# Optimization experiments

Measured on AMD Instinct MI355X. Metric: run time of the kernel, lower is better.

Reference implementation:

```python
import jax, jax.numpy as jnp
import numpy as np

N_P, N_W, F_IN = 512, 3584, 256
H1, O1 = 8, 32
H2, O2 = 8, 256
BATCH = 1024
NEG_SLOPE = 0.2


def _xavier(key, shape):
    fan_in, fan_out = shape[-2], shape[-1]
    lim = jnp.sqrt(6.0 / (fan_in + fan_out))
    return jax.random.uniform(key, shape, jnp.float32, -lim, lim)


def setup_inputs() -> dict:
    key = jax.random.key(0)
    ks = jax.random.split(key, 16)
    return {
        "input": jax.random.uniform(ks[0], (BATCH, N_W), jnp.float32),
        "pern_feature": jax.random.normal(ks[1], (N_P, F_IN), jnp.float32),
        "word_feature": jax.random.normal(ks[2], (N_W, F_IN), jnp.float32),
        "w1": _xavier(ks[3], (H1, F_IN, O1)),
        "a_src1": _xavier(ks[4], (H1, O1, 1)),
        "a_dst1": _xavier(ks[5], (H1, O1, 1)),
        "b1": jnp.zeros((O1,), jnp.float32),
        "w2": _xavier(ks[6], (H2, F_IN, O2)),
        "a_src2": _xavier(ks[7], (H2, F_IN, 1)),
        "a_dst2": _xavier(ks[8], (H2, F_IN, 1)),
        "b2": jnp.zeros((O2,), jnp.float32),
        "W_fc": _xavier(ks[9], (O2, 5)),
        "b_fc": jnp.zeros((5,), jnp.float32),
        "pern_adj": jax.random.randint(ks[10], (N_P, N_P), 0, 2, jnp.int32),
        "word_pern_adj": jax.random.randint(ks[11], (N_P + N_W, N_P + N_W), 0, 2, jnp.int32),
    }


def gat(h, adj, w, a_src, a_dst, bias):
    # h: [N, f_in], adj: [N, N] int, w: [H, f_in, f_out]
    h_prime = jnp.einsum('nf,hfo->hno', h, w)          # [H, N, O]
    t = jnp.tanh(h_prime)
    s_src = jnp.einsum('hno,hoi->hn', t, a_src)        # [H, N]
    s_dst = jnp.einsum('hno,hoi->hn', t, a_dst)        # [H, N]
    attn = s_src[:, :, None] + s_dst[:, None, :]       # [H, N, N]
    attn = jnp.where(attn >= 0, attn, NEG_SLOPE * attn)  # leaky_relu
    attn = jnp.where(adj[None, :, :] > 0, attn, -jnp.inf)
    attn = jax.nn.softmax(attn, axis=-1)
    out = jnp.einsum('hnm,hmo->hno', attn, h_prime)    # [H, N, O]
    return out + bias


def reference(input, pern_feature, word_feature, w1, a_src1, a_dst1, b1,
              w2, a_src2, a_dst2, b2, W_fc, b_fc, pern_adj, word_pern_adj):
    n_p = pern_feature.shape[0]
    # GAT 1 over personality graph
    h1 = gat(pern_feature, pern_adj, w1, a_src1, a_dst1, b1)       # [H1, n_p, O1]
    hiddn_pp = jnp.transpose(h1, (1, 0, 2)).reshape(n_p, -1)        # [n_p, H1*O1]
    hiddn_pp = jax.nn.elu(hiddn_pp)
    # dropout is identity in eval mode
    hiddn_wp = jnp.concatenate([word_feature, hiddn_pp], axis=0)    # [N, 256]
    h2 = gat(hiddn_wp, word_pern_adj, w2, a_src2, a_dst2, b2)       # [H2, N, O2]
    hiddn_wp2 = h2.mean(axis=0)                                     # [N, O2]
    hiddn_w = hiddn_wp2[:word_feature.shape[0], :]                  # [n_w, O2]
    x = (input @ hiddn_w) / input.sum(axis=1, keepdims=True)        # [B, O2]
    return x @ W_fc + b_fc                                          # [B, 5]
```

## Files before the change

### kernel.cpp

```cpp
#include <hip/hip_runtime.h>
#include <hip/hip_bf16.h>
#include <math.h>

#define NP 512
#define NW 3584
#define NT 4096
#define FIN 256
#define H1 8
#define O1 32
#define H2 8
#define O2 256
#define NEG 0.2f

typedef __attribute__((ext_vector_type(8))) short bf16x8;
typedef __attribute__((ext_vector_type(4))) float f32x4;
typedef __attribute__((ext_vector_type(2))) float v2f;
typedef unsigned long long u64;

__device__ __forceinline__ unsigned short f2bf(float f) {
    unsigned u = __float_as_uint(f);
    unsigned r = (u + 0x7FFF + ((u >> 16) & 1)) >> 16;
    return (unsigned short)r;
}
__device__ __forceinline__ float bf2f(unsigned short s) {
    return __uint_as_float(((unsigned)s) << 16);
}

__global__ __launch_bounds__(256) void k_prep(
    const float* __restrict__ wf, const float* __restrict__ pf,
    const float* __restrict__ w1, const float* __restrict__ a_src1,
    const float* __restrict__ a_dst1, const float* __restrict__ w2,
    const float* __restrict__ b2, const float* __restrict__ W_fc,
    const int* __restrict__ wp_adj,
    unsigned short* __restrict__ abf, unsigned short* __restrict__ btbf,
    float* __restrict__ hp1, float* __restrict__ ss1, float* __restrict__ sd1,
    u64* __restrict__ maskT64, float* __restrict__ cvec)
{
    __shared__ float tile[64][65];
    __shared__ float feat[2][FIN];
    __shared__ float red[4][5];
    int blk = blockIdx.x;
    int t = threadIdx.x;
    if (blk < 896) {
        int idx4 = blk * 256 + t;
        float4 x = ((const float4*)wf)[idx4];
        ushort4 y;
        y.x = f2bf(x.x); y.y = f2bf(x.y); y.z = f2bf(x.z); y.w = f2bf(x.w);
        ((ushort4*)abf)[idx4] = y;
    } else if (blk < 1152) {
        int n0 = (blk - 896) * 2;
        feat[0][t] = pf[n0 * FIN + t];
        feat[1][t] = pf[(n0 + 1) * FIN + t];
        __syncthreads();
        int h = t >> 5, o = t & 31;
        float acc0 = 0.f, acc1 = 0.f;
        const float* wcol = w1 + h * FIN * O1 + o;
        #pragma unroll 4
        for (int f = 0; f < FIN; f++) {
            float w = wcol[f * O1];
            acc0 += feat[0][f] * w;
            acc1 += feat[1][f] * w;
        }
        hp1[n0 * 256 + t] = acc0;
        hp1[(n0 + 1) * 256 + t] = acc1;
        float as = a_src1[h * O1 + o];
        float ad = a_dst1[h * O1 + o];
        float accs[2] = {acc0, acc1};
        #pragma unroll
        for (int i = 0; i < 2; i++) {
            float th = tanhf(accs[i]);
            float vs = th * as, vd = th * ad;
            #pragma unroll
            for (int off = 1; off < 32; off <<= 1) {
                vs += __shfl_xor(vs, off);
                vd += __shfl_xor(vd, off);
            }
            if (o == 0) { ss1[h * NP + n0 + i] = vs; sd1[h * NP + n0 + i] = vd; }
        }
    } else if (blk < 1280) {
        int blk2 = blk - 1152;
        int h = blk2 >> 4;
        int f0 = ((blk2 >> 2) & 3) * 64;
        int o0 = (blk2 & 3) * 64;
        #pragma unroll
        for (int rr = 0; rr < 16; rr++) {
            int f = rr * 4 + (t >> 6);
            int o = t & 63;
            tile[f][o] = w2[((size_t)(h * FIN + f0 + f)) * O2 + o0 + o];
        }
        __syncthreads();
        #pragma unroll
        for (int rr = 0; rr < 16; rr++) {
            int o = rr * 4 + (t >> 6);
            int f = t & 63;
            btbf[((size_t)(h * O2 + o0 + o)) * FIN + f0 + f] = f2bf(tile[f][o]);
        }
    } else if (blk < 2176) {
        int w = t >> 6, l = t & 63;
        int r = (blk - 1280) * 4 + w;
        const int4* row = (const int4*)(wp_adj + (size_t)r * NT);
        for (int c4 = 0; c4 < 16; c4++) {
            int4 x = row[c4 * 64 + l];
            u64 nib = (u64)((x.x != 0 ? 1 : 0) | (x.y != 0 ? 2 : 0) |
                            (x.z != 0 ? 4 : 0) | (x.w != 0 ? 8 : 0));
            u64 v = nib << (4 * (l & 15));
            v |= __shfl_xor(v, 1);
            v |= __shfl_xor(v, 2);
            v |= __shfl_xor(v, 4);
            v |= __shfl_xor(v, 8);
            if ((l & 15) == 0) {
                int qw = c4 * 4 + (l >> 4);
                maskT64[(size_t)qw * NW + r] = v;
            }
        }
    } else {
        float v[5];
        #pragma unroll
        for (int j = 0; j < 5; j++) v[j] = b2[t] * W_fc[t * 5 + j];
        #pragma unroll
        for (int off = 1; off < 64; off <<= 1)
            #pragma unroll
            for (int j = 0; j < 5; j++) v[j] += __shfl_xor(v[j], off);
        int w = t >> 6, l = t & 63;
        if (l == 0) { for (int j = 0; j < 5; j++) red[w][j] = v[j]; }
        __syncthreads();
        if (t == 0)
            for (int j = 0; j < 5; j++) cvec[j] = red[0][j] + red[1][j] + red[2][j] + red[3][j];
    }
}

__global__ __launch_bounds__(256) void k_gat1_attn(
    const int* __restrict__ adj, const float* __restrict__ hp1,
    const float* __restrict__ ss1, const float* __restrict__ sd1,
    const float* __restrict__ b1, unsigned short* __restrict__ abf)
{
    __shared__ float p[2][H1][NP];
    __shared__ float den[2][H1];
    int t = threadIdx.x;
    int n0 = blockIdx.x * 2;
    for (int rr = 0; rr < 32; rr++) {
        int idx = rr * 256 + t;
        int i = idx >> 12, h = (idx >> 9) & 7, m = idx & 511;
        float a = adj[(n0 + i) * NP + m] > 0 ? 1.0f : 0.0f;
        float e = ss1[h * NP + n0 + i] + sd1[h * NP + m];
        e = fmaxf(e, NEG * e);
        p[i][h][m] = a * __expf(e);
    }
    __syncthreads();
    int w = t >> 6, l = t & 63;
    {
        int i = w & 1;
        #pragma unroll
        for (int hh = 0; hh < 4; hh++) {
            int h = (w >> 1) * 4 + hh;
            float s = 0;
            #pragma unroll
            for (int q = 0; q < 8; q++) s += p[i][h][l + 64 * q];
            #pragma unroll
            for (int off = 1; off < 64; off <<= 1) s += __shfl_xor(s, off);
            if (l == 0) den[i][h] = s;
        }
    }
    __syncthreads();
    int h = t >> 5, o = t & 31;
    float a0a = 0.f, a0b = 0.f, a1a = 0.f, a1b = 0.f;
    #pragma unroll 8
    for (int m = 0; m < NP; m += 2) {
        float v0 = hp1[m * 256 + t];
        float v1 = hp1[(m + 1) * 256 + t];
        a0a += p[0][h][m] * v0;
        a1a += p[1][h][m] * v0;
        a0b += p[0][h][m + 1] * v1;
        a1b += p[1][h][m + 1] * v1;
    }
    float acc[2] = {a0a + a0b, a1a + a1b};
    float bo = b1[o];
    #pragma unroll
    for (int i = 0; i < 2; i++) {
        float r = acc[i] / den[i][h] + bo;
        r = r > 0.f ? r : expm1f(r);
        abf[(NW + n0 + i) * FIN + t] = f2bf(r);
    }
}

__global__ __launch_bounds__(256) void k_gemm_hp2(
    const unsigned short* __restrict__ abf, const unsigned short* __restrict__ btbf,
    unsigned short* __restrict__ hp2T)
{
    __shared__ unsigned short As[64][264];
    int b = blockIdx.x;
    int h = b & 7, mt = b >> 3;
    int t = threadIdx.x;
    int w = t >> 6, l = t & 63;
    int m0 = mt * 64;
    {
        int row = t >> 5;
        int col8 = (t & 31) * 8;
        #pragma unroll
        for (int u = 0; u < 8; u++)
            *(bf16x8*)(&As[u * 8 + row][col8]) =
                *(const bf16x8*)(abf + (size_t)(m0 + u * 8 + row) * FIN + col8);
    }
    __syncthreads();
    int n0 = w * 64;
    int lr = l & 15, lq = l >> 4;
    const unsigned short* bbase = btbf + h * O2 * FIN;
    f32x4 acc[4][4];
    #pragma unroll
    for (int i = 0; i < 4; i++)
        #pragma unroll
        for (int j = 0; j < 4; j++) acc[i][j] = (f32x4){0.f, 0.f, 0.f, 0.f};
    #pragma unroll
    for (int k = 0; k < FIN; k += 32) {
        bf16x8 a[4], bf[4];
        int kc = k + lq * 8;
        #pragma unroll
        for (int j = 0; j < 4; j++)
            bf[j] = *(const bf16x8*)(bbase + (size_t)(n0 + j * 16 + lr) * FIN + kc);
        #pragma unroll
        for (int i = 0; i < 4; i++)
            a[i] = *(const bf16x8*)(&As[i * 16 + lr][kc]);
        #pragma unroll
        for (int i = 0; i < 4; i++)
            #pragma unroll
            for (int j = 0; j < 4; j++)
                acc[i][j] = __builtin_amdgcn_mfma_f32_16x16x32_bf16(bf[j], a[i], acc[i][j], 0, 0, 0);
    }
    #pragma unroll
    for (int i = 0; i < 4; i++)
        #pragma unroll
        for (int j = 0; j < 4; j++)
            #pragma unroll
            for (int r = 0; r < 4; r++) {
                int o = n0 + j * 16 + lq * 4 + r;
                hp2T[((size_t)h * O2 + o) * NT + m0 + i * 16 + lr] = f2bf(acc[i][j][r]);
            }
}

__global__ __launch_bounds__(256) void k_reduce(
    const unsigned short* __restrict__ hp2T,
    const float* __restrict__ a_src2, const float* __restrict__ a_dst2,
    const float* __restrict__ W_fc, float* __restrict__ gpart)
{
    int b = blockIdx.x;
    int cs = b & 3, mb = (b >> 2) & 15, h = b >> 6;
    int m = mb * 256 + threadIdx.x;
    float s[7] = {0,0,0,0,0,0,0};
    const unsigned short* base = hp2T + ((size_t)h * O2 + cs * 64) * NT + m;
    #pragma unroll 8
    for (int oi = 0; oi < 64; oi++) {
        int o = cs * 64 + oi;
        float x = bf2f(base[(size_t)oi * NT]);
        float ex = __expf(2.0f * x);
        float th = 1.0f - 2.0f * __builtin_amdgcn_rcpf(ex + 1.0f);
        s[0] += th * a_src2[h * O2 + o];
        s[1] += th * a_dst2[h * O2 + o];
        #pragma unroll
        for (int jj = 0; jj < 5; jj++) s[2 + jj] += x * W_fc[o * 5 + jj];
    }
    float* dst = gpart + (((size_t)(h * 4 + cs)) * NT + m) * 8;
    float4 d0 = {s[0], s[1], s[2], s[3]};
    float4 d1 = {s[4], s[5], s[6], 0.f};
    *(float4*)dst = d0;
    *(float4*)(dst + 4) = d1;
}

__global__ __launch_bounds__(256) void k_comb_hp2(
    const float* __restrict__ gpart,
    float* __restrict__ Etab, float* __restrict__ Eptab, float* __restrict__ T)
{
    int idx = blockIdx.x * 256 + threadIdx.x;
    float s[7] = {0,0,0,0,0,0,0};
    #pragma unroll
    for (int sl = 0; sl < 4; sl++) {
        const float* p = gpart + (((size_t)(idx >> 12) * 4 + sl) * NT + (idx & (NT - 1))) * 8;
        #pragma unroll
        for (int q = 0; q < 7; q++) s[q] += p[q];
    }
    Etab[idx]  = __expf(s[0]);
    Eptab[idx] = __expf(NEG * s[0]);
    float4 t0 = {__expf(s[1]), __expf(NEG * s[1]), 1.0f, s[2]};
    float4 t1 = {s[3], s[4], s[5], s[6]};
    *(float4*)(T + (size_t)idx * 8)     = t0;
    *(float4*)(T + (size_t)idx * 8 + 4) = t1;
}

__global__ __launch_bounds__(256) void k_gat2_attn(
    const u64* __restrict__ maskT64, const float* __restrict__ Etab,
    const float* __restrict__ Eptab, const float* __restrict__ T,
    float* __restrict__ part)
{
    int t = threadIdx.x;
    int w = t >> 6, l = t & 63;
    int b = blockIdx.x;
    int nb = b % 112;
    int h  = (b / 112) & 7;
    int c  = b / 896;
    int n0 = __builtin_amdgcn_readfirstlane(nb * 32 + w * 8);
    u64 epk[8];
    #pragma unroll
    for (int i = 0; i < 8; i++) {
        int r = h * NT + n0 + i;
        unsigned e  = __builtin_amdgcn_readfirstlane(__float_as_uint(Etab[r]));
        unsigned ep = __builtin_amdgcn_readfirstlane(__float_as_uint(Eptab[r]));
        epk[i] = ((u64)ep << 32) | e;
    }
    float den[8] = {0,0,0,0,0,0,0,0};
    float num[8][5] = {{0}};
    const float* Th = T + ((size_t)h * NT + c * 2048) * 8;
    for (int q = 0; q < 32; q++) {
        const float* tp = Th + (size_t)(q * 64 + l) * 8;
        f32x4 t0 = *(const f32x4*)tp;
        f32x4 t1 = *(const f32x4*)(tp + 4);
        v2f ffp = {t0.x, t0.y};
        size_t moff = (size_t)(c * 32 + q) * NW + n0;
        const u64* mq = maskT64 + moff;
        #pragma unroll
        for (int i = 0; i < 8; i++) {
            u64 wv = mq[i];
            unsigned wlo = __builtin_amdgcn_readfirstlane((unsigned)wv);
            unsigned whi = __builtin_amdgcn_readfirstlane((unsigned)(wv >> 32));
            u64 word = ((u64)whi << 32) | wlo;
            v2f pab;
            asm("v_pk_mul_f32 %0, %1, %2" : "=v"(pab) : "v"(ffp), "s"(epk[i]));
            float pp0 = fmaxf(pab.x, pab.y);
            float pp;
            asm("v_cndmask_b32 %0, 0, %1, %2" : "=v"(pp) : "v"(pp0), "s"(word));
            den[i] += pp;
            num[i][0] = fmaf(pp, t0.w, num[i][0]);
            num[i][1] = fmaf(pp, t1.x, num[i][1]);
            num[i][2] = fmaf(pp, t1.y, num[i][2]);
            num[i][3] = fmaf(pp, t1.z, num[i][3]);
            num[i][4] = fmaf(pp, t1.w, num[i][4]);
        }
    }
    #pragma unroll
    for (int i = 0; i < 8; i++) {
        float v[6];
        v[0] = den[i];
        #pragma unroll
        for (int j = 0; j < 5; j++) v[1 + j] = num[i][j];
        #pragma unroll
        for (int off = 1; off < 8; off <<= 1)
            #pragma unroll
            for (int k = 0; k < 6; k++) v[k] += __shfl_xor(v[k], off);
        if ((l & 7) == 0) {
            float* dst = part + ((((size_t)c * NW + n0 + i) * 8 + h) * 8 + (l >> 3)) * 8;
            #pragma unroll
            for (int k = 0; k < 6; k++) dst[k] = v[k];
        }
    }
}

__global__ __launch_bounds__(256) void k_gat2_comb(const float* __restrict__ part,
                                                   float* __restrict__ hf) {
    int idx = blockIdx.x * 256 + threadIdx.x;
    int n = idx >> 3, h = idx & 7;
    float den = 0, num[5] = {0,0,0,0,0};
    #pragma unroll
    for (int cc = 0; cc < 2; cc++) {
        #pragma unroll
        for (int s = 0; s < 8; s++) {
            const float* p = part + ((((size_t)cc * NW + n) * 8 + h) * 8 + s) * 8;
            float4 a = *(const float4*)p;
            float4 bq = *(const float4*)(p + 4);
            den += a.x;
            num[0] += a.y; num[1] += a.z; num[2] += a.w;
            num[3] += bq.x; num[4] += bq.y;
        }
    }
    float inv = 1.0f / (den * 8.0f);
    float v[5];
    #pragma unroll
    for (int j = 0; j < 5; j++) v[j] = num[j] * inv;
    #pragma unroll
    for (int off = 1; off < 8; off <<= 1)
        #pragma unroll
        for (int j = 0; j < 5; j++) v[j] += __shfl_xor(v[j], off);
    if (h == 0) {
        #pragma unroll
        for (int j = 0; j < 5; j++) hf[n * 5 + j] = v[j];
    }
}

__global__ __launch_bounds__(256) void k_final(
    const float* __restrict__ input, const float* __restrict__ hf,
    const float* __restrict__ cvec, const float* __restrict__ b_fc,
    float* __restrict__ out)
{
    int b = blockIdx.x, t = threadIdx.x;
    const float4* row4 = (const float4*)(input + (size_t)b * NW);
    const float4* hf4 = (const float4*)hf;
    float s = 0.f, a[5] = {0.f, 0.f, 0.f, 0.f, 0.f};
    for (int idx = t; idx < NW / 4; idx += 256) {
        float4 x = row4[idx];
        float f[20];
        #pragma unroll
        for (int q = 0; q < 5; q++) *(float4*)(f + 4 * q) = hf4[idx * 5 + q];
        s += x.x + x.y + x.z + x.w;
        #pragma unroll
        for (int j = 0; j < 5; j++)
            a[j] += x.x * f[j] + x.y * f[5 + j] + x.z * f[10 + j] + x.w * f[15 + j];
    }
    #pragma unroll
    for (int off = 1; off < 64; off <<= 1) {
        s += __shfl_xor(s, off);
        #pragma unroll
        for (int j = 0; j < 5; j++) a[j] += __shfl_xor(a[j], off);
    }
    __shared__ float red[4][6];
    int w = t >> 6, l = t & 63;
    if (l == 0) { red[w][0] = s; for (int j = 0; j < 5; j++) red[w][j + 1] = a[j]; }
    __syncthreads();
    if (t < 5) {
        float st = red[0][0] + red[1][0] + red[2][0] + red[3][0];
        float aj = red[0][t + 1] + red[1][t + 1] + red[2][t + 1] + red[3][t + 1];
        out[b * 5 + t] = aj / st + cvec[t] + b_fc[t];
    }
}

extern "C" void kernel_launch(void* const* d_in, const int* in_sizes, int n_in,
                              void* d_out, int out_size, void* d_ws, size_t ws_size,
                              hipStream_t stream) {
    const float* input   = (const float*)d_in[0];
    const float* pf      = (const float*)d_in[1];
    const float* wf      = (const float*)d_in[2];
    const float* w1      = (const float*)d_in[3];
    const float* a_src1  = (const float*)d_in[4];
    const float* a_dst1  = (const float*)d_in[5];
    const float* b1      = (const float*)d_in[6];
    const float* w2      = (const float*)d_in[7];
    const float* a_src2  = (const float*)d_in[8];
    const float* a_dst2  = (const float*)d_in[9];
    const float* b2      = (const float*)d_in[10];
    const float* W_fc    = (const float*)d_in[11];
    const float* b_fc    = (const float*)d_in[12];
    const int* pern_adj  = (const int*)d_in[13];
    const int* wp_adj    = (const int*)d_in[14];
    float* out = (float*)d_out;

    char* ws = (char*)d_ws;
    unsigned short* abf    = (unsigned short*)(ws);
    unsigned short* btbf   = (unsigned short*)(ws + 2097152);
    float*          hp1    = (float*)(ws + 3145728);
    float*          ss1    = (float*)(ws + 3670016);
    float*          sd1    = (float*)(ws + 3686400);
    float*          Etab   = (float*)(ws + 3833856);
    float*          Eptab  = (float*)(ws + 3964928);
    float*          T      = (float*)(ws + 4096000);
    float*          hf     = (float*)(ws + 5144576);
    float*          cvec   = (float*)(ws + 5216256);
    u64*            maskT64= (u64*)(ws + 5216512);
    float*          gpart  = (float*)(ws + 7051520);
    unsigned short* hp2T   = (unsigned short*)(ws + 11245824);
    float*          part   = (float*)(ws + 11245824);

    k_prep<<<2177, 256, 0, stream>>>(wf, pf, w1, a_src1, a_dst1, w2, b2, W_fc,
                                     wp_adj, abf, btbf, hp1, ss1, sd1, maskT64, cvec);
    k_gat1_attn<<<256, 256, 0, stream>>>(pern_adj, hp1, ss1, sd1, b1, abf);
    k_gemm_hp2<<<512, 256, 0, stream>>>(abf, btbf, hp2T);
    k_reduce<<<512, 256, 0, stream>>>(hp2T, a_src2, a_dst2, W_fc, gpart);
    k_comb_hp2<<<128, 256, 0, stream>>>(gpart, Etab, Eptab, T);
    k_gat2_attn<<<1792, 256, 0, stream>>>(maskT64, Etab, Eptab, T, part);
    k_gat2_comb<<<112, 256, 0, stream>>>(part, hf);
    k_final<<<1024, 256, 0, stream>>>(input, hf, cvec, b_fc, out);
}
```

Before: 250.7 us.

## Fuse tanh/score reduction into GEMM epilogue and stage adjacency mask in LDS

The separate k_reduce pass is folded into the hp2 GEMM epilogue. The epilogue computes the tanh attention scores and the W_fc projections straight from the MFMA accumulators, which drops the bf16 hp2T round trip through global memory and one kernel launch. A small weight table packs a_src2, a_dst2 and W_fc per output column. The GAT2 attention kernel now reads the adjacency mask as 32-bit words staged in shared memory, extracting bits per lane instead of using readfirstlane and an inline-asm cndmask on 64-bit words. This adds some shuffle reductions in the epilogue, and per-lane bit extraction costs extra VALU work in the hot loop.

Measured after the change: 248.3 us. About the same (-1.0%).

```diff
diff --git a/kernel.cpp b/kernel.cpp
--- a/kernel.cpp
+++ b/kernel.cpp
@@ -14,7 +14,6 @@
 
 typedef __attribute__((ext_vector_type(8))) short bf16x8;
 typedef __attribute__((ext_vector_type(4))) float f32x4;
-typedef __attribute__((ext_vector_type(2))) float v2f;
 typedef unsigned long long u64;
 
 __device__ __forceinline__ unsigned short f2bf(float f) {
@@ -22,8 +21,8 @@
     unsigned r = (u + 0x7FFF + ((u >> 16) & 1)) >> 16;
     return (unsigned short)r;
 }
-__device__ __forceinline__ float bf2f(unsigned short s) {
-    return __uint_as_float(((unsigned)s) << 16);
+__device__ __forceinline__ float rflf(float x) {
+    return __uint_as_float(__builtin_amdgcn_readfirstlane(__float_as_uint(x)));
 }
 
 __global__ __launch_bounds__(256) void k_prep(
@@ -31,10 +30,12 @@
     const float* __restrict__ w1, const float* __restrict__ a_src1,
     const float* __restrict__ a_dst1, const float* __restrict__ w2,
     const float* __restrict__ b2, const float* __restrict__ W_fc,
+    const float* __restrict__ a_src2, const float* __restrict__ a_dst2,
     const int* __restrict__ wp_adj,
     unsigned short* __restrict__ abf, unsigned short* __restrict__ btbf,
     float* __restrict__ hp1, float* __restrict__ ss1, float* __restrict__ sd1,
-    u64* __restrict__ maskT64, float* __restrict__ cvec)
+    unsigned* __restrict__ maskT, float* __restrict__ cvec,
+    float* __restrict__ wtab)
 {
     __shared__ float tile[64][65];
     __shared__ float feat[2][FIN];
@@ -110,10 +111,11 @@
             v |= __shfl_xor(v, 8);
             if ((l & 15) == 0) {
                 int qw = c4 * 4 + (l >> 4);
-                maskT64[(size_t)qw * NW + r] = v;
+                maskT[(size_t)(2 * qw) * NW + r]     = (unsigned)v;
+                maskT[(size_t)(2 * qw + 1) * NW + r] = (unsigned)(v >> 32);
             }
         }
-    } else {
+    } else if (blk == 2176) {
         float v[5];
         #pragma unroll
         for (int j = 0; j < 5; j++) v[j] = b2[t] * W_fc[t * 5 + j];
@@ -126,6 +128,14 @@
         __syncthreads();
         if (t == 0)
             for (int j = 0; j < 5; j++) cvec[j] = red[0][j] + red[1][j] + red[2][j] + red[3][j];
+    } else {
+        int h = blk - 2177;
+        int o = t;
+        float* dst = wtab + ((size_t)h * O2 + o) * 8;
+        float4 d0 = {a_src2[h * O2 + o], a_dst2[h * O2 + o], W_fc[o * 5], W_fc[o * 5 + 1]};
+        float4 d1 = {W_fc[o * 5 + 2], W_fc[o * 5 + 3], W_fc[o * 5 + 4], 0.f};
+        *(float4*)dst = d0;
+        *(float4*)(dst + 4) = d1;
     }
 }
 
@@ -185,7 +195,7 @@
 
 __global__ __launch_bounds__(256) void k_gemm_hp2(
     const unsigned short* __restrict__ abf, const unsigned short* __restrict__ btbf,
-    unsigned short* __restrict__ hp2T)
+    const float* __restrict__ wtab, float* __restrict__ gpart)
 {
     __shared__ unsigned short As[64][264];
     int b = blockIdx.x;
@@ -226,43 +236,42 @@
             for (int j = 0; j < 4; j++)
                 acc[i][j] = __builtin_amdgcn_mfma_f32_16x16x32_bf16(bf[j], a[i], acc[i][j], 0, 0, 0);
     }
-    #pragma unroll
-    for (int i = 0; i < 4; i++)
-        #pragma unroll
-        for (int j = 0; j < 4; j++)
+    const float* wt = wtab + (size_t)h * O2 * 8;
+    float* base = gpart + ((size_t)h * 4 + w) * NT * 8;
+    #pragma unroll
+    for (int i = 0; i < 4; i++) {
+        float s[7] = {0,0,0,0,0,0,0};
+        #pragma unroll
+        for (int j = 0; j < 4; j++) {
             #pragma unroll
             for (int r = 0; r < 4; r++) {
-                int o = n0 + j * 16 + lq * 4 + r;
-                hp2T[((size_t)h * O2 + o) * NT + m0 + i * 16 + lr] = f2bf(acc[i][j][r]);
+                float x = acc[i][j][r];
+                float ex = __expf(2.0f * x);
+                float th = 1.0f - 2.0f * __builtin_amdgcn_rcpf(ex + 1.0f);
+                const float* wp = wt + (size_t)(n0 + j * 16 + lq * 4 + r) * 8;
+                float4 wa = *(const float4*)wp;
+                float4 wb = *(const float4*)(wp + 4);
+                s[0] += th * wa.x;
+                s[1] += th * wa.y;
+                s[2] += x * wa.z;
+                s[3] += x * wa.w;
+                s[4] += x * wb.x;
+                s[5] += x * wb.y;
+                s[6] += x * wb.z;
             }
-}
-
-__global__ __launch_bounds__(256) void k_reduce(
-    const unsigned short* __restrict__ hp2T,
-    const float* __restrict__ a_src2, const float* __restrict__ a_dst2,
-    const float* __restrict__ W_fc, float* __restrict__ gpart)
-{
-    int b = blockIdx.x;
-    int cs = b & 3, mb = (b >> 2) & 15, h = b >> 6;
-    int m = mb * 256 + threadIdx.x;
-    float s[7] = {0,0,0,0,0,0,0};
-    const unsigned short* base = hp2T + ((size_t)h * O2 + cs * 64) * NT + m;
-    #pragma unroll 8
-    for (int oi = 0; oi < 64; oi++) {
-        int o = cs * 64 + oi;
-        float x = bf2f(base[(size_t)oi * NT]);
-        float ex = __expf(2.0f * x);
-        float th = 1.0f - 2.0f * __builtin_amdgcn_rcpf(ex + 1.0f);
-        s[0] += th * a_src2[h * O2 + o];
-        s[1] += th * a_dst2[h * O2 + o];
-        #pragma unroll
-        for (int jj = 0; jj < 5; jj++) s[2 + jj] += x * W_fc[o * 5 + jj];
-    }
-    float* dst = gpart + (((size_t)(h * 4 + cs)) * NT + m) * 8;
-    float4 d0 = {s[0], s[1], s[2], s[3]};
-    float4 d1 = {s[4], s[5], s[6], 0.f};
-    *(float4*)dst = d0;
-    *(float4*)(dst + 4) = d1;
+        }
+        #pragma unroll
+        for (int q = 0; q < 7; q++) {
+            s[q] += __shfl_xor(s[q], 16);
+            s[q] += __shfl_xor(s[q], 32);
+        }
+        if (lq == 0) {
+            int m = m0 + i * 16 + lr;
+            float* dst = base + (size_t)m * 8;
+            #pragma unroll
+            for (int q = 0; q < 7; q++) dst[q] = s[q];
+        }
+    }
 }
 
 __global__ __launch_bounds__(256) void k_comb_hp2(
@@ -286,46 +295,53 @@
 }
 
 __global__ __launch_bounds__(256) void k_gat2_attn(
-    const u64* __restrict__ maskT64, const float* __restrict__ Etab,
+    const unsigned* __restrict__ maskT, const float* __restrict__ Etab,
     const float* __restrict__ Eptab, const float* __restrict__ T,
     float* __restrict__ part)
 {
+    __shared__ unsigned pw[64 * 32];
     int t = threadIdx.x;
     int w = t >> 6, l = t & 63;
     int b = blockIdx.x;
     int nb = b % 112;
     int h  = (b / 112) & 7;
     int c  = b / 896;
-    int n0 = __builtin_amdgcn_readfirstlane(nb * 32 + w * 8);
-    u64 epk[8];
+    int rbase = nb * 32;
+    #pragma unroll
+    for (int u = 0; u < 8; u++) {
+        int idx = u * 256 + t;
+        int wd = idx >> 5, row = idx & 31;
+        pw[idx] = maskT[(size_t)(c * 64 + wd) * NW + rbase + row];
+    }
+    __syncthreads();
+    int n0 = rbase + w * 8;
+    float E[8], Ep[8];
     #pragma unroll
     for (int i = 0; i < 8; i++) {
         int r = h * NT + n0 + i;
-        unsigned e  = __builtin_amdgcn_readfirstlane(__float_as_uint(Etab[r]));
-        unsigned ep = __builtin_amdgcn_readfirstlane(__float_as_uint(Eptab[r]));
-        epk[i] = ((u64)ep << 32) | e;
+        E[i]  = rflf(Etab[r]);
+        Ep[i] = rflf(Eptab[r]);
     }
     float den[8] = {0,0,0,0,0,0,0,0};
     float num[8][5] = {{0}};
     const float* Th = T + ((size_t)h * NT + c * 2048) * 8;
+    int lsh = l & 31;
+    int wdh = l >> 5;
+    const unsigned* mbase = pw + w * 8;
     for (int q = 0; q < 32; q++) {
         const float* tp = Th + (size_t)(q * 64 + l) * 8;
         f32x4 t0 = *(const f32x4*)tp;
         f32x4 t1 = *(const f32x4*)(tp + 4);
-        v2f ffp = {t0.x, t0.y};
-        size_t moff = (size_t)(c * 32 + q) * NW + n0;
-        const u64* mq = maskT64 + moff;
+        int wd = q * 2 + wdh;
+        uint4 ma = *(const uint4*)(mbase + wd * 32);
+        uint4 mb = *(const uint4*)(mbase + wd * 32 + 4);
+        unsigned wv[8] = {ma.x, ma.y, ma.z, ma.w, mb.x, mb.y, mb.z, mb.w};
         #pragma unroll
         for (int i = 0; i < 8; i++) {
-            u64 wv = mq[i];
-            unsigned wlo = __builtin_amdgcn_readfirstlane((unsigned)wv);
-            unsigned whi = __builtin_amdgcn_readfirstlane((unsigned)(wv >> 32));
-            u64 word = ((u64)whi << 32) | wlo;
-            v2f pab;
-            asm("v_pk_mul_f32 %0, %1, %2" : "=v"(pab) : "v"(ffp), "s"(epk[i]));
-            float pp0 = fmaxf(pab.x, pab.y);
-            float pp;
-            asm("v_cndmask_b32 %0, 0, %1, %2" : "=v"(pp) : "v"(pp0), "s"(word));
+            float bm = (float)((wv[i] >> lsh) & 1u);
+            float pa = t0.x * E[i];
+            float pb = t0.y * Ep[i];
+            float pp = fmaxf(pa, pb) * bm;
             den[i] += pp;
             num[i][0] = fmaf(pp, t0.w, num[i][0]);
             num[i][1] = fmaf(pp, t1.x, num[i][1]);
@@ -450,18 +466,18 @@
     float*          T      = (float*)(ws + 4096000);
     float*          hf     = (float*)(ws + 5144576);
     float*          cvec   = (float*)(ws + 5216256);
-    u64*            maskT64= (u64*)(ws + 5216512);
+    unsigned*       maskT  = (unsigned*)(ws + 5216512);
     float*          gpart  = (float*)(ws + 7051520);
-    unsigned short* hp2T   = (unsigned short*)(ws + 11245824);
     float*          part   = (float*)(ws + 11245824);
-
-    k_prep<<<2177, 256, 0, stream>>>(wf, pf, w1, a_src1, a_dst1, w2, b2, W_fc,
-                                     wp_adj, abf, btbf, hp1, ss1, sd1, maskT64, cvec);
+    float*          wtab   = (float*)(ws + 26214400);
+
+    k_prep<<<2185, 256, 0, stream>>>(wf, pf, w1, a_src1, a_dst1, w2, b2, W_fc,
+                                     a_src2, a_dst2, wp_adj,
+                                     abf, btbf, hp1, ss1, sd1, maskT, cvec, wtab);
     k_gat1_attn<<<256, 256, 0, stream>>>(pern_adj, hp1, ss1, sd1, b1, abf);
-    k_gemm_hp2<<<512, 256, 0, stream>>>(abf, btbf, hp2T);
-    k_reduce<<<512, 256, 0, stream>>>(hp2T, a_src2, a_dst2, W_fc, gpart);
+    k_gemm_hp2<<<512, 256, 0, stream>>>(abf, btbf, wtab, gpart);
     k_comb_hp2<<<128, 256, 0, stream>>>(gpart, Etab, Eptab, T);
-    k_gat2_attn<<<1792, 256, 0, stream>>>(maskT64, Etab, Eptab, T, part);
+    k_gat2_attn<<<1792, 256, 0, stream>>>(maskT, Etab, Eptab, T, part);
     k_gat2_comb<<<112, 256, 0, stream>>>(part, hf);
     k_final<<<1024, 256, 0, stream>>>(input, hf, cvec, b_fc, out);
 }
```
